# Optimization experiments

Measured on AMD Instinct MI355X. Metric: run time of the kernel, lower is better.

Reference implementation:

```python
import jax, jax.numpy as jnp
import numpy as np

N, E, B = 200000, 6400000, 128
IN_LOCAL, IN_GLOBAL, HIDDEN, NUM_CLASSES = 16, 8, 32, 2


def setup_inputs() -> dict:
    key = jax.random.key(0)
    ks = jax.random.split(key, 16)
    inp = {
        "x_local": jax.random.normal(ks[0], (N, IN_LOCAL), dtype=jnp.float32),
        "x_global": jax.random.normal(ks[1], (B, IN_GLOBAL), dtype=jnp.float32),
        "batch": jnp.sort(jax.random.randint(ks[2], (N,), 0, B, dtype=jnp.int64)),
        "edge_index": jax.random.randint(ks[3], (2, E), 0, N, dtype=jnp.int64),
        # encoder params
        "W_local": jax.random.normal(ks[4], (IN_LOCAL, HIDDEN), jnp.float32) / np.sqrt(IN_LOCAL),
        "b_local": jnp.zeros((HIDDEN,), jnp.float32),
        "W_global": jax.random.normal(ks[5], (IN_GLOBAL, HIDDEN), jnp.float32) / np.sqrt(IN_GLOBAL),
        "b_global": jnp.zeros((HIDDEN,), jnp.float32),
        "W_mix": jax.random.normal(ks[6], (3 * HIDDEN, HIDDEN), jnp.float32) / np.sqrt(3 * HIDDEN),
        "b_mix": jnp.zeros((HIDDEN,), jnp.float32),
        # GNN layer params
        "W_msg": jax.random.normal(ks[7], (HIDDEN, HIDDEN), jnp.float32) / np.sqrt(HIDDEN),
        "b_msg": jnp.zeros((HIDDEN,), jnp.float32),
        "W_self": jax.random.normal(ks[8], (HIDDEN, HIDDEN), jnp.float32) / np.sqrt(HIDDEN),
        "b_self": jnp.zeros((HIDDEN,), jnp.float32),
        # output head
        "W_out": jax.random.normal(ks[9], (HIDDEN, NUM_CLASSES), jnp.float32) / np.sqrt(HIDDEN),
        "b_out": jnp.zeros((NUM_CLASSES,), jnp.float32),
    }
    return inp


def reference(x_local, x_global, batch, edge_index,
              W_local, b_local, W_global, b_global, W_mix, b_mix,
              W_msg, b_msg, W_self, b_self, W_out, b_out):
    n = x_local.shape[0]
    # --- MixedSelectivityNodeEncoder ---
    h_local = jax.nn.relu(x_local @ W_local + b_local)            # [N,H]
    h_global_graph = jax.nn.relu(x_global @ W_global + b_global)  # [B,H]
    h_global = h_global_graph[batch]                              # gather -> [N,H]
    h_int = h_local * h_global
    h_cat = jnp.concatenate([h_local, h_global, h_int], axis=-1)  # [N,3H]
    h0 = jax.nn.relu(h_cat @ W_mix + b_mix)                       # [N,H]
    # --- GNN layer with self loops, add aggregation ---
    loops = jnp.arange(n, dtype=edge_index.dtype)
    src = jnp.concatenate([edge_index[0], loops])                 # [E+N]
    dst = jnp.concatenate([edge_index[1], loops])                 # [E+N]
    msg = jax.nn.relu(h0[src] @ W_msg + b_msg)                    # [E+N,H]
    aggr = jax.ops.segment_sum(msg, dst, num_segments=n)          # [N,H]
    h = jax.nn.relu(aggr + h0 @ W_self + b_self)                  # [N,H]
    # --- output head ---
    return h @ W_out + b_out                                      # [N,C]
```

## Files before the change

### kernel.cpp

```cpp
#include <hip/hip_runtime.h>

#define N_NODES  200000
#define N_EDGES  6400000
#define NGRAPH   128
#define H        32

#define BNODES   256
#define NBUCK    782
#define P_BLOCKS 256
#define EPB      25000
#define ENC_BLOCKS 782
#define SORT_CAP 8960


typedef unsigned short ushort_t;

__device__ __forceinline__ ushort_t f32_to_bf16_rne(float f) {
    unsigned u = __float_as_uint(f);
    unsigned r = (u + 0x7fffu + ((u >> 16) & 1u)) >> 16;
    return (ushort_t)r;
}
__device__ __forceinline__ float bf16_to_f32(ushort_t h) {
    return __uint_as_float(((unsigned)h) << 16);
}

__global__ __launch_bounds__(256, 1) void k_enc_part(
        const float* __restrict__ xl,
        const int*   __restrict__ batch,
        const float* __restrict__ xg,   const float* __restrict__ Wg,
        const float* __restrict__ bg,
        const float* __restrict__ Wl,   const float* __restrict__ bl,
        const float* __restrict__ Wmix, const float* __restrict__ bmix,
        const float* __restrict__ Wmsg, const float* __restrict__ bmsg,
        const float* __restrict__ Wself,const float* __restrict__ bself,
        ushort_t* __restrict__ mb, float* __restrict__ s,
        const int* __restrict__ ei,
        int* __restrict__ gcur,
        unsigned int* __restrict__ ebuf) {
    __shared__ int cnt[NBUCK];
    __shared__ int basex[NBUCK];
    int tid = threadIdx.x;

    if (blockIdx.x >= ENC_BLOCKS) {
        int blk = blockIdx.x - ENC_BLOCKS;
        for (int i = tid; i < NBUCK; i += 256) cnt[i] = 0;
        __syncthreads();

        int e0 = blk * EPB, e1 = e0 + EPB;
        for (int e = e0 + tid; e < e1; e += 256)
            atomicAdd(&cnt[ei[N_EDGES + e] >> 8], 1);
        __syncthreads();

        for (int i = tid; i < NBUCK; i += 256) {
            int c = cnt[i];
            basex[i] = (c > 0) ? atomicAdd(&gcur[i * 32], c) : 0;
        }
        __syncthreads();

        for (int e = e0 + tid; e < e1; e += 256) {
            unsigned src = (unsigned)ei[e];
            int dst = ei[N_EDGES + e];
            int bkt = dst >> 8;
            int pos = atomicAdd(&basex[bkt], 1);
            if (pos < SORT_CAP)
                ebuf[(size_t)bkt * SORT_CAP + pos] = (src << 8) | (unsigned)(dst & 255);
        }
        return;
    }

    int n0 = blockIdx.x * 256 + tid;
    bool valid = (n0 < N_NODES);
    int n = valid ? n0 : (N_NODES - 1);

    float xv[16];
    {
        const float4* p = (const float4*)(xl + (size_t)n * 16);
        float4 a = p[0], b = p[1], c = p[2], d = p[3];
        xv[0]=a.x; xv[1]=a.y; xv[2]=a.z; xv[3]=a.w;
        xv[4]=b.x; xv[5]=b.y; xv[6]=b.z; xv[7]=b.w;
        xv[8]=c.x; xv[9]=c.y; xv[10]=c.z; xv[11]=c.w;
        xv[12]=d.x; xv[13]=d.y; xv[14]=d.z; xv[15]=d.w;
    }
    float gvv[8];
    {
        int gb = batch[n];
        const float4* q = (const float4*)(xg + (size_t)gb * 8);
        float4 a = q[0], b = q[1];
        gvv[0]=a.x; gvv[1]=a.y; gvv[2]=a.z; gvv[3]=a.w;
        gvv[4]=b.x; gvv[5]=b.y; gvv[6]=b.z; gvv[7]=b.w;
    }

    float4 acc4[8];
#pragma unroll
    for (int t4 = 0; t4 < 8; ++t4) acc4[t4] = ((const float4*)bmix)[t4];

#pragma unroll
    for (int k = 0; k < 32; ++k) {
        float hlk = bl[k];
#pragma unroll
        for (int j = 0; j < 16; ++j)
            hlk = fmaf(xv[j], Wl[j * H + k], hlk);
        hlk = fmaxf(hlk, 0.f);
        float hgk = bg[k];
#pragma unroll
        for (int j = 0; j < 8; ++j)
            hgk = fmaf(gvv[j], Wg[j * H + k], hgk);
        hgk = fmaxf(hgk, 0.f);
        float hik = hlk * hgk;
#pragma unroll
        for (int t4 = 0; t4 < 8; ++t4) {
            float4 w1 = ((const float4*)(Wmix + k * H))[t4];
            float4 w2 = ((const float4*)(Wmix + (32 + k) * H))[t4];
            float4 w3 = ((const float4*)(Wmix + (64 + k) * H))[t4];
            acc4[t4].x = fmaf(hlk, w1.x, fmaf(hgk, w2.x, fmaf(hik, w3.x, acc4[t4].x)));
            acc4[t4].y = fmaf(hlk, w1.y, fmaf(hgk, w2.y, fmaf(hik, w3.y, acc4[t4].y)));
            acc4[t4].z = fmaf(hlk, w1.z, fmaf(hgk, w2.z, fmaf(hik, w3.z, acc4[t4].z)));
            acc4[t4].w = fmaf(hlk, w1.w, fmaf(hgk, w2.w, fmaf(hik, w3.w, acc4[t4].w)));
        }
    }

    float h0[32];
#pragma unroll
    for (int t4 = 0; t4 < 8; ++t4) {
        h0[t4*4+0] = fmaxf(acc4[t4].x, 0.f); h0[t4*4+1] = fmaxf(acc4[t4].y, 0.f);
        h0[t4*4+2] = fmaxf(acc4[t4].z, 0.f); h0[t4*4+3] = fmaxf(acc4[t4].w, 0.f);
    }

#pragma unroll
    for (int t4 = 0; t4 < 8; ++t4) {
        float4 am = ((const float4*)bmsg)[t4];
#pragma unroll
        for (int k = 0; k < 32; ++k) {
            float4 wm = ((const float4*)(Wmsg + k * H))[t4];
            am.x = fmaf(h0[k], wm.x, am.x); am.y = fmaf(h0[k], wm.y, am.y);
            am.z = fmaf(h0[k], wm.z, am.z); am.w = fmaf(h0[k], wm.w, am.w);
        }
        if (valid) {
            unsigned d0 = (unsigned)f32_to_bf16_rne(fmaxf(am.x, 0.f))
                        | ((unsigned)f32_to_bf16_rne(fmaxf(am.y, 0.f)) << 16);
            unsigned d1 = (unsigned)f32_to_bf16_rne(fmaxf(am.z, 0.f))
                        | ((unsigned)f32_to_bf16_rne(fmaxf(am.w, 0.f)) << 16);
            ((unsigned*)(mb + (size_t)n * H))[t4*2+0] = d0;
            ((unsigned*)(mb + (size_t)n * H))[t4*2+1] = d1;
        }
    }

#pragma unroll
    for (int t4 = 0; t4 < 8; ++t4) {
        float4 as = ((const float4*)bself)[t4];
#pragma unroll
        for (int k = 0; k < 32; ++k) {
            float4 ws = ((const float4*)(Wself + k * H))[t4];
            as.x = fmaf(h0[k], ws.x, as.x); as.y = fmaf(h0[k], ws.y, as.y);
            as.z = fmaf(h0[k], ws.z, as.z); as.w = fmaf(h0[k], ws.w, as.w);
        }
        if (valid)
            ((float4*)(s + (size_t)n * H))[t4] = as;
    }
}

__global__ __launch_bounds__(512, 8) void k_bsort_aggr(
        const int* __restrict__ gcur,
        const unsigned int* __restrict__ ebuf,
        const ushort_t* __restrict__ mb, const float* __restrict__ s,
        const float* __restrict__ Wout, const float* __restrict__ bout,
        float* __restrict__ out) {
    __shared__ unsigned sorted[SORT_CAP];
    __shared__ int cnt[BNODES];
    __shared__ int offx[BNODES + 1];
    __shared__ int cur[BNODES];
    __shared__ int wsum[4];
    int tid = threadIdx.x, b = blockIdx.x;

    size_t base = (size_t)b * SORT_CAP;
    int sz = min(gcur[b * 32], SORT_CAP);

    if (tid < BNODES) cnt[tid] = 0;
    __syncthreads();

    for (int j = tid; j < sz; j += 512)
        atomicAdd(&cnt[ebuf[base + j] & 255], 1);
    __syncthreads();

    {
        int lane = tid & 63, w = tid >> 6;
        int v = (tid < BNODES) ? cnt[tid] : 0;
#pragma unroll
        for (int d = 1; d < 64; d <<= 1) {
            int u = __shfl_up(v, d, 64);
            if (lane >= d) v += u;
        }
        if (tid < BNODES && lane == 63) wsum[w] = v;
        __syncthreads();
        if (tid < BNODES) {
            int add = 0;
#pragma unroll
            for (int i = 0; i < 3; ++i) add += (i < w) ? wsum[i] : 0;
            int inc = v + add;
            offx[tid + 1] = inc;
            cur[tid] = inc - cnt[tid];
            if (tid == 0) offx[0] = 0;
        }
        __syncthreads();
    }

    for (int j = tid; j < sz; j += 512) {
        unsigned pk = ebuf[base + j];
        int pos = atomicAdd(&cur[pk & 255], 1);
        sorted[pos] = pk;
    }
    __syncthreads();

    const unsigned* mb32 = (const unsigned*)mb;
    int g = tid >> 4;
    int t = tid & 15;

    for (int q = 0; q < 8; ++q) {
        int loc = (g << 3) + q;
        int n = b * BNODES + loc;
        int rs = offx[loc];
        int re = offx[loc + 1];
        float a0 = 0.f, a1 = 0.f;

        for (int j = rs; j < re; j += 8) {
            unsigned pk[8], u[8];
#pragma unroll
            for (int k = 0; k < 8; ++k)
                pk[k] = sorted[min(j + k, re - 1)];
#pragma unroll
            for (int k = 0; k < 8; ++k)
                u[k] = mb32[(pk[k] >> 8) * 16u + (unsigned)t];
#pragma unroll
            for (int k = 0; k < 8; ++k) {
                bool ok = (j + k < re);
                a0 += ok ? __uint_as_float(u[k] << 16)         : 0.f;
                a1 += ok ? __uint_as_float(u[k] & 0xffff0000u) : 0.f;
            }
        }

        if (n < N_NODES) {
            unsigned u = mb32[(unsigned)n * 16u + (unsigned)t];
            float2 sv = *(const float2*)(s + (size_t)n * H + 2 * t);
            float h0 = fmaxf(a0 + __uint_as_float(u << 16)         + sv.x, 0.f);
            float h1 = fmaxf(a1 + __uint_as_float(u & 0xffff0000u) + sv.y, 0.f);
            float4 w = *(const float4*)(Wout + 4 * t);
            float p0 = h0 * w.x + h1 * w.z;
            float p1 = h0 * w.y + h1 * w.w;
#pragma unroll
            for (int o = 8; o >= 1; o >>= 1) {
                p0 += __shfl_down(p0, o, 16);
                p1 += __shfl_down(p1, o, 16);
            }
            if (t == 0) {
                float2 o2;
                o2.x = p0 + bout[0];
                o2.y = p1 + bout[1];
                *(float2*)(out + (size_t)n * 2) = o2;
            }
        }
    }
}

extern "C" void kernel_launch(void* const* d_in, const int* in_sizes, int n_in,
                              void* d_out, int out_size, void* d_ws, size_t ws_size,
                              hipStream_t stream) {
    const float* xl    = (const float*)d_in[0];
    const float* xg    = (const float*)d_in[1];
    const int*   batch = (const int*)  d_in[2];
    const int*   ei    = (const int*)  d_in[3];
    const float* Wl    = (const float*)d_in[4];
    const float* bl    = (const float*)d_in[5];
    const float* Wg    = (const float*)d_in[6];
    const float* bg    = (const float*)d_in[7];
    const float* Wmix  = (const float*)d_in[8];
    const float* bmix  = (const float*)d_in[9];
    const float* Wmsg  = (const float*)d_in[10];
    const float* bmsg  = (const float*)d_in[11];
    const float* Wself = (const float*)d_in[12];
    const float* bself = (const float*)d_in[13];
    const float* Wout  = (const float*)d_in[14];
    const float* bout  = (const float*)d_in[15];
    float* out = (float*)d_out;

    float*    s    = (float*)d_ws;
    ushort_t* mb   = (ushort_t*)(s + (size_t)N_NODES * H);
    int*      gcur = (int*)(mb + (size_t)N_NODES * H);
    unsigned int* ebuf = (unsigned int*)(gcur + (size_t)NBUCK * 32);

    hipMemsetAsync(gcur, 0, (size_t)NBUCK * 32 * sizeof(int), stream);

    k_enc_part<<<ENC_BLOCKS + P_BLOCKS, 256, 0, stream>>>(
        xl, batch, xg, Wg, bg, Wl, bl, Wmix, bmix,
        Wmsg, bmsg, Wself, bself, mb, s,
        ei, gcur, ebuf);

    k_bsort_aggr<<<NBUCK, 512, 0, stream>>>(gcur, ebuf, mb, s, Wout, bout, out);
}
```

Measured before the change: 436.8 us.

## Split fused encoder/partition kernel into separate encoder stages and partition kernel

The single kernel that ran the node encoder and the edge bucket partition in different blocks is split into three kernels. The encoder becomes two kernels with h0 staged through global memory in the edge buffer, and the partition gets its own 1024-thread kernel. This is meant to relieve register pressure and the launch_bounds(256,1) occupancy limit of the fused kernel. The cost is the lost overlap between encoder and partition work, plus extra global traffic to write and reread h0 (about 25.6 MB) and two more launches.

```diff
diff --git a/kernel.cpp b/kernel.cpp
--- a/kernel.cpp
+++ b/kernel.cpp
@@ -9,7 +9,6 @@
 #define NBUCK    782
 #define P_BLOCKS 256
 #define EPB      25000
-#define ENC_BLOCKS 782
 #define SORT_CAP 8960
 
 
@@ -24,51 +23,15 @@
     return __uint_as_float(((unsigned)h) << 16);
 }
 
-__global__ __launch_bounds__(256, 1) void k_enc_part(
+__global__ __launch_bounds__(256) void k_enc_h0(
         const float* __restrict__ xl,
         const int*   __restrict__ batch,
         const float* __restrict__ xg,   const float* __restrict__ Wg,
         const float* __restrict__ bg,
         const float* __restrict__ Wl,   const float* __restrict__ bl,
         const float* __restrict__ Wmix, const float* __restrict__ bmix,
-        const float* __restrict__ Wmsg, const float* __restrict__ bmsg,
-        const float* __restrict__ Wself,const float* __restrict__ bself,
-        ushort_t* __restrict__ mb, float* __restrict__ s,
-        const int* __restrict__ ei,
-        int* __restrict__ gcur,
-        unsigned int* __restrict__ ebuf) {
-    __shared__ int cnt[NBUCK];
-    __shared__ int basex[NBUCK];
-    int tid = threadIdx.x;
-
-    if (blockIdx.x >= ENC_BLOCKS) {
-        int blk = blockIdx.x - ENC_BLOCKS;
-        for (int i = tid; i < NBUCK; i += 256) cnt[i] = 0;
-        __syncthreads();
-
-        int e0 = blk * EPB, e1 = e0 + EPB;
-        for (int e = e0 + tid; e < e1; e += 256)
-            atomicAdd(&cnt[ei[N_EDGES + e] >> 8], 1);
-        __syncthreads();
-
-        for (int i = tid; i < NBUCK; i += 256) {
-            int c = cnt[i];
-            basex[i] = (c > 0) ? atomicAdd(&gcur[i * 32], c) : 0;
-        }
-        __syncthreads();
-
-        for (int e = e0 + tid; e < e1; e += 256) {
-            unsigned src = (unsigned)ei[e];
-            int dst = ei[N_EDGES + e];
-            int bkt = dst >> 8;
-            int pos = atomicAdd(&basex[bkt], 1);
-            if (pos < SORT_CAP)
-                ebuf[(size_t)bkt * SORT_CAP + pos] = (src << 8) | (unsigned)(dst & 255);
-        }
-        return;
-    }
-
-    int n0 = blockIdx.x * 256 + tid;
+        float* __restrict__ h0buf) {
+    int n0 = blockIdx.x * 256 + threadIdx.x;
     bool valid = (n0 < N_NODES);
     int n = valid ? n0 : (N_NODES - 1);
 
@@ -119,11 +82,31 @@
         }
     }
 
+    if (valid) {
+#pragma unroll
+        for (int t4 = 0; t4 < 8; ++t4) {
+            float4 h;
+            h.x = fmaxf(acc4[t4].x, 0.f); h.y = fmaxf(acc4[t4].y, 0.f);
+            h.z = fmaxf(acc4[t4].z, 0.f); h.w = fmaxf(acc4[t4].w, 0.f);
+            ((float4*)(h0buf + (size_t)n * H))[t4] = h;
+        }
+    }
+}
+
+__global__ __launch_bounds__(256) void k_enc_out(
+        const float* __restrict__ h0buf,
+        const float* __restrict__ Wmsg, const float* __restrict__ bmsg,
+        const float* __restrict__ Wself,const float* __restrict__ bself,
+        ushort_t* __restrict__ mb, float* __restrict__ s) {
+    int n0 = blockIdx.x * 256 + threadIdx.x;
+    bool valid = (n0 < N_NODES);
+    int n = valid ? n0 : (N_NODES - 1);
+
     float h0[32];
 #pragma unroll
     for (int t4 = 0; t4 < 8; ++t4) {
-        h0[t4*4+0] = fmaxf(acc4[t4].x, 0.f); h0[t4*4+1] = fmaxf(acc4[t4].y, 0.f);
-        h0[t4*4+2] = fmaxf(acc4[t4].z, 0.f); h0[t4*4+3] = fmaxf(acc4[t4].w, 0.f);
+        float4 h = ((const float4*)(h0buf + (size_t)n * H))[t4];
+        h0[t4*4+0] = h.x; h0[t4*4+1] = h.y; h0[t4*4+2] = h.z; h0[t4*4+3] = h.w;
     }
 
 #pragma unroll
@@ -156,6 +139,37 @@
         }
         if (valid)
             ((float4*)(s + (size_t)n * H))[t4] = as;
+    }
+}
+
+__global__ __launch_bounds__(1024) void k_ppart(
+        const int* __restrict__ ei,
+        int* __restrict__ gcur,
+        unsigned int* __restrict__ ebuf) {
+    __shared__ int cnt[NBUCK];
+    __shared__ int basex[NBUCK];
+    int t = threadIdx.x, blk = blockIdx.x;
+    for (int i = t; i < NBUCK; i += 1024) cnt[i] = 0;
+    __syncthreads();
+
+    int e0 = blk * EPB, e1 = e0 + EPB;
+    for (int e = e0 + t; e < e1; e += 1024)
+        atomicAdd(&cnt[ei[N_EDGES + e] >> 8], 1);
+    __syncthreads();
+
+    for (int i = t; i < NBUCK; i += 1024) {
+        int c = cnt[i];
+        basex[i] = (c > 0) ? atomicAdd(&gcur[i * 32], c) : 0;
+    }
+    __syncthreads();
+
+    for (int e = e0 + t; e < e1; e += 1024) {
+        unsigned src = (unsigned)ei[e];
+        int dst = ei[N_EDGES + e];
+        int bkt = dst >> 8;
+        int pos = atomicAdd(&basex[bkt], 1);
+        if (pos < SORT_CAP)
+            ebuf[(size_t)bkt * SORT_CAP + pos] = (src << 8) | (unsigned)(dst & 255);
     }
 }
 
@@ -286,13 +300,15 @@
     ushort_t* mb   = (ushort_t*)(s + (size_t)N_NODES * H);
     int*      gcur = (int*)(mb + (size_t)N_NODES * H);
     unsigned int* ebuf = (unsigned int*)(gcur + (size_t)NBUCK * 32);
+    float*    h0buf = (float*)ebuf;
+
+    k_enc_h0<<<(N_NODES + 255) / 256, 256, 0, stream>>>(
+        xl, batch, xg, Wg, bg, Wl, bl, Wmix, bmix, h0buf);
+
+    k_enc_out<<<(N_NODES + 255) / 256, 256, 0, stream>>>(
+        h0buf, Wmsg, bmsg, Wself, bself, mb, s);
 
     hipMemsetAsync(gcur, 0, (size_t)NBUCK * 32 * sizeof(int), stream);
-
-    k_enc_part<<<ENC_BLOCKS + P_BLOCKS, 256, 0, stream>>>(
-        xl, batch, xg, Wg, bg, Wl, bl, Wmix, bmix,
-        Wmsg, bmsg, Wself, bself, mb, s,
-        ei, gcur, ebuf);
-
+    k_ppart<<<P_BLOCKS, 1024, 0, stream>>>(ei, gcur, ebuf);
     k_bsort_aggr<<<NBUCK, 512, 0, stream>>>(gcur, ebuf, mb, s, Wout, bout, out);
 }
```

After: 386.2 us. 1.13x faster.

## Split encoder and edge partition into separate kernels, stage weights in LDS

Applied to the files above, without the earlier changes.

The fused encoder-plus-partition kernel is split in two. The encoder kernel now copies all weight matrices into shared memory, with W_local and W_global transposed for vectorized reads, and computes the msg and self projections in one loop. Edge partitioning moves to its own kernel with 1024-thread blocks. This aims to cut scalar global/constant weight loads and to tune each phase separately, at the cost of one extra launch and losing the overlap of the encoder and partition work inside a single grid.

```diff
diff --git a/kernel.cpp b/kernel.cpp
--- a/kernel.cpp
+++ b/kernel.cpp
@@ -9,7 +9,6 @@
 #define NBUCK    782
 #define P_BLOCKS 256
 #define EPB      25000
-#define ENC_BLOCKS 782
 #define SORT_CAP 8960
 
 
@@ -24,7 +23,7 @@
     return __uint_as_float(((unsigned)h) << 16);
 }
 
-__global__ __launch_bounds__(256, 1) void k_enc_part(
+__global__ __launch_bounds__(256, 1) void k_enc_lds(
         const float* __restrict__ xl,
         const int*   __restrict__ batch,
         const float* __restrict__ xg,   const float* __restrict__ Wg,
@@ -33,40 +32,28 @@
         const float* __restrict__ Wmix, const float* __restrict__ bmix,
         const float* __restrict__ Wmsg, const float* __restrict__ bmsg,
         const float* __restrict__ Wself,const float* __restrict__ bself,
-        ushort_t* __restrict__ mb, float* __restrict__ s,
-        const int* __restrict__ ei,
-        int* __restrict__ gcur,
-        unsigned int* __restrict__ ebuf) {
-    __shared__ int cnt[NBUCK];
-    __shared__ int basex[NBUCK];
+        ushort_t* __restrict__ mb, float* __restrict__ s) {
+    __shared__ __attribute__((aligned(16))) float wl_t[32 * 16];
+    __shared__ __attribute__((aligned(16))) float wg_t[32 * 8];
+    __shared__ __attribute__((aligned(16))) float wmixL[96 * 32];
+    __shared__ __attribute__((aligned(16))) float wmsgL[32 * 32];
+    __shared__ __attribute__((aligned(16))) float wselfL[32 * 32];
+    __shared__ __attribute__((aligned(16))) float bL[32];
+    __shared__ __attribute__((aligned(16))) float bG[32];
+    __shared__ __attribute__((aligned(16))) float bM[32];
+    __shared__ __attribute__((aligned(16))) float bMs[32];
+    __shared__ __attribute__((aligned(16))) float bSf[32];
     int tid = threadIdx.x;
 
-    if (blockIdx.x >= ENC_BLOCKS) {
-        int blk = blockIdx.x - ENC_BLOCKS;
-        for (int i = tid; i < NBUCK; i += 256) cnt[i] = 0;
-        __syncthreads();
-
-        int e0 = blk * EPB, e1 = e0 + EPB;
-        for (int e = e0 + tid; e < e1; e += 256)
-            atomicAdd(&cnt[ei[N_EDGES + e] >> 8], 1);
-        __syncthreads();
-
-        for (int i = tid; i < NBUCK; i += 256) {
-            int c = cnt[i];
-            basex[i] = (c > 0) ? atomicAdd(&gcur[i * 32], c) : 0;
-        }
-        __syncthreads();
-
-        for (int e = e0 + tid; e < e1; e += 256) {
-            unsigned src = (unsigned)ei[e];
-            int dst = ei[N_EDGES + e];
-            int bkt = dst >> 8;
-            int pos = atomicAdd(&basex[bkt], 1);
-            if (pos < SORT_CAP)
-                ebuf[(size_t)bkt * SORT_CAP + pos] = (src << 8) | (unsigned)(dst & 255);
-        }
-        return;
-    }
+    for (int i = tid; i < 512; i += 256)  wl_t[i] = Wl[(i & 15) * H + (i >> 4)];
+    for (int i = tid; i < 256; i += 256)  wg_t[i] = Wg[(i & 7) * H + (i >> 3)];
+    for (int i = tid; i < 3072; i += 256) wmixL[i] = Wmix[i];
+    for (int i = tid; i < 1024; i += 256) { wmsgL[i] = Wmsg[i]; wselfL[i] = Wself[i]; }
+    if (tid < 32) {
+        bL[tid] = bl[tid]; bG[tid] = bg[tid]; bM[tid] = bmix[tid];
+        bMs[tid] = bmsg[tid]; bSf[tid] = bself[tid];
+    }
+    __syncthreads();
 
     int n0 = blockIdx.x * 256 + tid;
     bool valid = (n0 < N_NODES);
@@ -92,26 +79,38 @@
 
     float4 acc4[8];
 #pragma unroll
-    for (int t4 = 0; t4 < 8; ++t4) acc4[t4] = ((const float4*)bmix)[t4];
+    for (int t4 = 0; t4 < 8; ++t4) acc4[t4] = ((const float4*)bM)[t4];
 
 #pragma unroll
     for (int k = 0; k < 32; ++k) {
-        float hlk = bl[k];
-#pragma unroll
-        for (int j = 0; j < 16; ++j)
-            hlk = fmaf(xv[j], Wl[j * H + k], hlk);
+        const float4* wr = (const float4*)(wl_t + k * 16);
+        float4 wa = wr[0], wb = wr[1], wc = wr[2], wd = wr[3];
+        float hlk = bL[k];
+        hlk = fmaf(xv[0], wa.x, hlk);  hlk = fmaf(xv[1], wa.y, hlk);
+        hlk = fmaf(xv[2], wa.z, hlk);  hlk = fmaf(xv[3], wa.w, hlk);
+        hlk = fmaf(xv[4], wb.x, hlk);  hlk = fmaf(xv[5], wb.y, hlk);
+        hlk = fmaf(xv[6], wb.z, hlk);  hlk = fmaf(xv[7], wb.w, hlk);
+        hlk = fmaf(xv[8], wc.x, hlk);  hlk = fmaf(xv[9], wc.y, hlk);
+        hlk = fmaf(xv[10], wc.z, hlk); hlk = fmaf(xv[11], wc.w, hlk);
+        hlk = fmaf(xv[12], wd.x, hlk); hlk = fmaf(xv[13], wd.y, hlk);
+        hlk = fmaf(xv[14], wd.z, hlk); hlk = fmaf(xv[15], wd.w, hlk);
         hlk = fmaxf(hlk, 0.f);
-        float hgk = bg[k];
-#pragma unroll
-        for (int j = 0; j < 8; ++j)
-            hgk = fmaf(gvv[j], Wg[j * H + k], hgk);
+
+        const float4* gr = (const float4*)(wg_t + k * 8);
+        float4 ga = gr[0], gb4 = gr[1];
+        float hgk = bG[k];
+        hgk = fmaf(gvv[0], ga.x, hgk);  hgk = fmaf(gvv[1], ga.y, hgk);
+        hgk = fmaf(gvv[2], ga.z, hgk);  hgk = fmaf(gvv[3], ga.w, hgk);
+        hgk = fmaf(gvv[4], gb4.x, hgk); hgk = fmaf(gvv[5], gb4.y, hgk);
+        hgk = fmaf(gvv[6], gb4.z, hgk); hgk = fmaf(gvv[7], gb4.w, hgk);
         hgk = fmaxf(hgk, 0.f);
+
         float hik = hlk * hgk;
 #pragma unroll
         for (int t4 = 0; t4 < 8; ++t4) {
-            float4 w1 = ((const float4*)(Wmix + k * H))[t4];
-            float4 w2 = ((const float4*)(Wmix + (32 + k) * H))[t4];
-            float4 w3 = ((const float4*)(Wmix + (64 + k) * H))[t4];
+            float4 w1 = ((const float4*)(wmixL + k * H))[t4];
+            float4 w2 = ((const float4*)(wmixL + (32 + k) * H))[t4];
+            float4 w3 = ((const float4*)(wmixL + (64 + k) * H))[t4];
             acc4[t4].x = fmaf(hlk, w1.x, fmaf(hgk, w2.x, fmaf(hik, w3.x, acc4[t4].x)));
             acc4[t4].y = fmaf(hlk, w1.y, fmaf(hgk, w2.y, fmaf(hik, w3.y, acc4[t4].y)));
             acc4[t4].z = fmaf(hlk, w1.z, fmaf(hgk, w2.z, fmaf(hik, w3.z, acc4[t4].z)));
@@ -119,21 +118,23 @@
         }
     }
 
-    float h0[32];
+    float* h0p = (float*)acc4;
+#pragma unroll
+    for (int i = 0; i < 32; ++i) h0p[i] = fmaxf(h0p[i], 0.f);
+
 #pragma unroll
     for (int t4 = 0; t4 < 8; ++t4) {
-        h0[t4*4+0] = fmaxf(acc4[t4].x, 0.f); h0[t4*4+1] = fmaxf(acc4[t4].y, 0.f);
-        h0[t4*4+2] = fmaxf(acc4[t4].z, 0.f); h0[t4*4+3] = fmaxf(acc4[t4].w, 0.f);
-    }
-
-#pragma unroll
-    for (int t4 = 0; t4 < 8; ++t4) {
-        float4 am = ((const float4*)bmsg)[t4];
+        float4 am = ((const float4*)bMs)[t4];
+        float4 as = ((const float4*)bSf)[t4];
 #pragma unroll
         for (int k = 0; k < 32; ++k) {
-            float4 wm = ((const float4*)(Wmsg + k * H))[t4];
-            am.x = fmaf(h0[k], wm.x, am.x); am.y = fmaf(h0[k], wm.y, am.y);
-            am.z = fmaf(h0[k], wm.z, am.z); am.w = fmaf(h0[k], wm.w, am.w);
+            float h0k = h0p[k];
+            float4 wm = ((const float4*)(wmsgL + k * H))[t4];
+            float4 ws = ((const float4*)(wselfL + k * H))[t4];
+            am.x = fmaf(h0k, wm.x, am.x); am.y = fmaf(h0k, wm.y, am.y);
+            am.z = fmaf(h0k, wm.z, am.z); am.w = fmaf(h0k, wm.w, am.w);
+            as.x = fmaf(h0k, ws.x, as.x); as.y = fmaf(h0k, ws.y, as.y);
+            as.z = fmaf(h0k, ws.z, as.z); as.w = fmaf(h0k, ws.w, as.w);
         }
         if (valid) {
             unsigned d0 = (unsigned)f32_to_bf16_rne(fmaxf(am.x, 0.f))
@@ -142,20 +143,39 @@
                         | ((unsigned)f32_to_bf16_rne(fmaxf(am.w, 0.f)) << 16);
             ((unsigned*)(mb + (size_t)n * H))[t4*2+0] = d0;
             ((unsigned*)(mb + (size_t)n * H))[t4*2+1] = d1;
-        }
-    }
-
-#pragma unroll
-    for (int t4 = 0; t4 < 8; ++t4) {
-        float4 as = ((const float4*)bself)[t4];
-#pragma unroll
-        for (int k = 0; k < 32; ++k) {
-            float4 ws = ((const float4*)(Wself + k * H))[t4];
-            as.x = fmaf(h0[k], ws.x, as.x); as.y = fmaf(h0[k], ws.y, as.y);
-            as.z = fmaf(h0[k], ws.z, as.z); as.w = fmaf(h0[k], ws.w, as.w);
-        }
-        if (valid)
             ((float4*)(s + (size_t)n * H))[t4] = as;
+        }
+    }
+}
+
+__global__ __launch_bounds__(1024) void k_ppart(
+        const int* __restrict__ ei,
+        int* __restrict__ gcur,
+        unsigned int* __restrict__ ebuf) {
+    __shared__ int cnt[NBUCK];
+    __shared__ int basex[NBUCK];
+    int t = threadIdx.x, blk = blockIdx.x;
+    for (int i = t; i < NBUCK; i += 1024) cnt[i] = 0;
+    __syncthreads();
+
+    int e0 = blk * EPB, e1 = e0 + EPB;
+    for (int e = e0 + t; e < e1; e += 1024)
+        atomicAdd(&cnt[ei[N_EDGES + e] >> 8], 1);
+    __syncthreads();
+
+    for (int i = t; i < NBUCK; i += 1024) {
+        int c = cnt[i];
+        basex[i] = (c > 0) ? atomicAdd(&gcur[i * 32], c) : 0;
+    }
+    __syncthreads();
+
+    for (int e = e0 + t; e < e1; e += 1024) {
+        unsigned src = (unsigned)ei[e];
+        int dst = ei[N_EDGES + e];
+        int bkt = dst >> 8;
+        int pos = atomicAdd(&basex[bkt], 1);
+        if (pos < SORT_CAP)
+            ebuf[(size_t)bkt * SORT_CAP + pos] = (src << 8) | (unsigned)(dst & 255);
     }
 }
 
@@ -287,12 +307,11 @@
     int*      gcur = (int*)(mb + (size_t)N_NODES * H);
     unsigned int* ebuf = (unsigned int*)(gcur + (size_t)NBUCK * 32);
 
+    k_enc_lds<<<(N_NODES + 255) / 256, 256, 0, stream>>>(
+        xl, batch, xg, Wg, bg, Wl, bl, Wmix, bmix,
+        Wmsg, bmsg, Wself, bself, mb, s);
+
     hipMemsetAsync(gcur, 0, (size_t)NBUCK * 32 * sizeof(int), stream);
-
-    k_enc_part<<<ENC_BLOCKS + P_BLOCKS, 256, 0, stream>>>(
-        xl, batch, xg, Wg, bg, Wl, bl, Wmix, bmix,
-        Wmsg, bmsg, Wself, bself, mb, s,
-        ei, gcur, ebuf);
-
+    k_ppart<<<P_BLOCKS, 1024, 0, stream>>>(ei, gcur, ebuf);
     k_bsort_aggr<<<NBUCK, 512, 0, stream>>>(gcur, ebuf, mb, s, Wout, bout, out);
 }
```

New measurement: 465.5 us. +6.6%, slower.
